# Performance work log

Hardware: AMD Instinct MI355X
Metric: run time of the kernel (lower is better)

## Reference

```python
import jax, jax.numpy as jnp
import numpy as np

N, E, B, IN, H = 20000, 50000, 1024, 32, 64

def setup_inputs() -> dict:
    key = jax.random.key(0)
    ks = jax.random.split(key, 32)
    d = {}
    d["x"] = jax.random.normal(ks[0], (N, IN), jnp.float32)
    d["edge_index"] = jax.random.randint(ks[1], (2, E), 0, N)
    d["edge_attr"] = jax.random.uniform(ks[2], (E, 6), dtype=jnp.float32)
    d["batch"] = jnp.sort(jax.random.randint(ks[3], (N,), 0, B))
    d["t"] = jax.random.uniform(ks[4], (B, 1), dtype=jnp.float32)
    d["p"] = jax.random.uniform(ks[5], (B, 1), dtype=jnp.float32)
    d["num_graphs"] = B
    def lin(k, fan_in, shape):
        return jax.random.normal(k, shape, jnp.float32) * (1.0 / np.sqrt(fan_in))
    # lin0: IN -> H
    d["W0"] = lin(ks[6], IN, (IN, H)); d["b0"] = jnp.zeros((H,), jnp.float32)
    # edge MLP: 6 -> 64 -> H*H
    d["We1"] = lin(ks[7], 6, (6, 64)); d["be1"] = jnp.zeros((64,), jnp.float32)
    d["We2"] = lin(ks[8], 64, (64, H * H)); d["be2"] = jnp.zeros((H * H,), jnp.float32)
    # NNConv root weight + bias
    d["Wroot"] = lin(ks[9], H, (H, H)); d["bconv"] = jnp.zeros((H,), jnp.float32)
    # GRU (input H, hidden H), torch layout [3H, *] gate order r,z,n
    d["gru_wih"] = lin(ks[10], H, (3 * H, H)); d["gru_whh"] = lin(ks[11], H, (3 * H, H))
    d["gru_bih"] = jnp.zeros((3 * H,), jnp.float32); d["gru_bhh"] = jnp.zeros((3 * H,), jnp.float32)
    # Set2Set LSTM (input 2H, hidden H), torch layout [4H, *] gate order i,f,g,o
    d["l_wih"] = lin(ks[12], 2 * H, (4 * H, 2 * H)); d["l_whh"] = lin(ks[13], H, (4 * H, H))
    d["l_bih"] = jnp.zeros((4 * H,), jnp.float32); d["l_bhh"] = jnp.zeros((4 * H,), jnp.float32)
    # readout MLP
    d["W1"] = lin(ks[14], 2 * H + 2, (2 * H + 2, H)); d["b1"] = jnp.zeros((H,), jnp.float32)
    d["W2"] = lin(ks[15], H, (H, 64)); d["b2"] = jnp.zeros((64,), jnp.float32)
    d["W3"] = lin(ks[16], 64, (64, 1)); d["b3"] = jnp.zeros((1,), jnp.float32)
    return d


def reference(x, edge_attr, t, p, W0, b0, We1, be1, We2, be2, Wroot, bconv,
              gru_wih, gru_whh, gru_bih, gru_bhh, l_wih, l_whh, l_bih, l_bhh,
              W1, b1, W2, b2, W3, b3, edge_index, batch, num_graphs):
    n_nodes = x.shape[0]
    hdim = W0.shape[1]
    src, dst = edge_index[0], edge_index[1]

    out = jax.nn.relu(x @ W0 + b0)            # [N,H]
    h = out

    # edge MLP -> per-edge weight matrices [E,H,H] (edge_attr is loop-invariant)
    ew = (jax.nn.relu(edge_attr @ We1 + be1) @ We2 + be2).reshape(-1, hdim, hdim)

    for _ in range(4):
        # NNConv: gather source features, per-edge matmul, scatter-add to targets
        msg = jnp.einsum('eh,eho->eo', out[src], ew)                 # [E,H]
        agg = jax.ops.segment_sum(msg, dst, num_segments=n_nodes)    # [N,H]
        m = jax.nn.relu(agg + out @ Wroot + bconv)
        # GRU step (single timestep)
        gi = m @ gru_wih.T + gru_bih
        gh = h @ gru_whh.T + gru_bhh
        ir, iz, inn = jnp.split(gi, 3, axis=-1)
        hr, hz, hn = jnp.split(gh, 3, axis=-1)
        r = jax.nn.sigmoid(ir + hr)
        z = jax.nn.sigmoid(iz + hz)
        nn_ = jnp.tanh(inn + r * hn)
        h = (1.0 - z) * nn_ + z * h
        out = h

    # Set2Set pooling, 3 processing steps
    qh = jnp.zeros((num_graphs, hdim), x.dtype)
    qc = jnp.zeros((num_graphs, hdim), x.dtype)
    q_star = jnp.zeros((num_graphs, 2 * hdim), x.dtype)
    for _ in range(3):
        g = q_star @ l_wih.T + l_bih + qh @ l_whh.T + l_bhh
        gi_, gf_, gg_, go_ = jnp.split(g, 4, axis=-1)
        qc = jax.nn.sigmoid(gf_) * qc + jax.nn.sigmoid(gi_) * jnp.tanh(gg_)
        qh = jax.nn.sigmoid(go_) * jnp.tanh(qc)
        q = qh                                                        # [B,H]
        e = jnp.sum(out * q[batch], axis=-1, keepdims=True)          # [N,1]
        emax = jax.ops.segment_max(e, batch, num_segments=num_graphs)
        a = jnp.exp(e - emax[batch])
        asum = jax.ops.segment_sum(a, batch, num_segments=num_graphs)
        a = a / asum[batch]                                           # segment softmax
        r_ = jax.ops.segment_sum(a * out, batch, num_segments=num_graphs)
        q_star = jnp.concatenate([q, r_], axis=-1)

    feat = jnp.concatenate([q_star, t, p], axis=-1)                   # [B,2H+2]
    y = jax.nn.relu(feat @ W1 + b1)
    y = jax.nn.relu(y @ W2 + b2)
    y = y @ W3 + b3
    return y.reshape(-1)
```

## Files before the change

kernel.cpp:

```cpp
#include <hip/hip_runtime.h>
#include <math.h>

#define N_NODES 20000
#define N_EDGES 50000
#define NB      1024
#define IND     32
#define HDIM    64

typedef __attribute__((ext_vector_type(8))) short bf16x8;
typedef __attribute__((ext_vector_type(4))) float f32x4;

static inline size_t align_up(size_t x, size_t a) { return (x + a - 1) & ~(a - 1); }

__device__ __forceinline__ float sigmoidf_(float x) {
    return 1.0f / (1.0f + __expf(-x));
}
__device__ __forceinline__ float tanhf_(float x) {
    float xc = fminf(fmaxf(x, -15.0f), 15.0f);
    float e = __expf(2.0f * xc);
    return (e - 1.0f) / (e + 1.0f);
}
__device__ __forceinline__ unsigned pk2(float p0, float p1) {
    unsigned u0 = __float_as_uint(p0) + 0x8000u;
    unsigned u1 = __float_as_uint(p1) + 0x8000u;
    return __builtin_amdgcn_perm(u1, u0, 0x07060302u);
}
__device__ __forceinline__ unsigned bf1(float v) {
    return (__float_as_uint(v) + 0x8000u) >> 16;
}

__global__ void k_prep(const float* __restrict__ We2, const float* __restrict__ be2,
                       short* __restrict__ We2b,
                       const float* __restrict__ Wroot, const float* __restrict__ gwhh,
                       const float* __restrict__ gwih,
                       short* __restrict__ WB1h, short* __restrict__ WB1l,
                       short* __restrict__ WB2h, short* __restrict__ WB2l,
                       const float* __restrict__ lwih, const float* __restrict__ lwhh,
                       float* __restrict__ lwihT, float* __restrict__ lwhhT,
                       const int* __restrict__ batch, int* __restrict__ offs,
                       const float* __restrict__ x, const float* __restrict__ W0,
                       const float* __restrict__ b0, float* __restrict__ hbuf,
                       const float* __restrict__ ea, const float* __restrict__ We1,
                       const float* __restrict__ be1, float* __restrict__ re,
                       const int* __restrict__ ei, int* __restrict__ deg) {
    int bid = blockIdx.x, tid = threadIdx.x;
    if (bid < 1040) {
        int idx = bid * 256 + tid;
        int s = idx >> 12;
        int col = idx & 4095;
        int k = col >> 6, o = col & 63;
        float val = (s < 64) ? We2[k * 4096 + s * 64 + o] : be2[k * 64 + o];
        int dst = s * 4096 + (((o >> 4) * 128 + (k >> 5) * 64 + ((k >> 3) & 3) * 16 + (o & 15)) << 3) + (k & 7);
        We2b[dst] = (short)bf1(val);
    } else if (bid < 1152) {
        int idx = (bid - 1040) * 256 + tid;
        if (idx < 28672) {
            bool b1 = idx < 16384;
            int li = b1 ? idx : idx - 16384;
            int j = li & 7, lane = (li >> 3) & 63, c = (li >> 9) & 1, otile = li >> 10;
            int k = c * 32 + (lane >> 4) * 8 + j;
            int o = otile * 16 + (lane & 15);
            float val;
            if (b1) val = (o < 64) ? Wroot[k * 64 + o] : gwhh[(o - 64) * 64 + k];
            else    val = gwih[o * 64 + k];
            unsigned hs = bf1(val);
            float lo = val - __uint_as_float(hs << 16);
            unsigned ls = bf1(lo);
            if (b1) { WB1h[li] = (short)hs; WB1l[li] = (short)ls; }
            else    { WB2h[li] = (short)hs; WB2l[li] = (short)ls; }
        }
    } else if (bid < 1280) {
        int idx = (bid - 1152) * 256 + tid;
        int i = idx >> 8, j = idx & 255;
        lwihT[idx] = lwih[j * 128 + i];
    } else if (bid < 1344) {
        int idx = (bid - 1280) * 256 + tid;
        int i = idx >> 8, j = idx & 255;
        lwhhT[idx] = lwhh[j * 64 + i];
    } else if (bid < 1349) {
        int i = (bid - 1344) * 256 + tid;
        if (i <= NB) {
            int lo = 0, hi = N_NODES;
            while (lo < hi) { int mid = (lo + hi) >> 1; if (batch[mid] < i) lo = mid + 1; else hi = mid; }
            offs[i] = lo;
        }
    } else if (bid < 6349) {
        int w = tid >> 6, j = tid & 63;
        int n = (bid - 1349) * 4 + w;
        float acc = b0[j];
        const float* xr = x + n * IND;
#pragma unroll
        for (int i = 0; i < IND; ++i) acc = fmaf(xr[i], W0[i * 64 + j], acc);
        hbuf[n * 64 + j] = fmaxf(acc, 0.0f);
    } else if (bid < 18849) {
        int w = tid >> 6, j = tid & 63;
        int e = (bid - 6349) * 4 + w;
        if (e < N_EDGES) {
            float acc = be1[j];
            const float* er = ea + e * 6;
#pragma unroll
            for (int i = 0; i < 6; ++i) acc = fmaf(er[i], We1[i * 64 + j], acc);
            re[e * 64 + j] = fmaxf(acc, 0.0f);
        }
    } else {
        int e = (bid - 18849) * 256 + tid;
        if (e < N_EDGES) atomicAdd(&deg[ei[N_EDGES + e]], 1);
    }
}

__global__ void k_scan(const int* __restrict__ deg, int* __restrict__ rowptr, int* __restrict__ cursor) {
    __shared__ int s_w[16];
    int t = threadIdx.x;
    int base = t * 20;
    int v[20]; int s = 0;
#pragma unroll
    for (int i = 0; i < 20; ++i) {
        int idx = base + i;
        v[i] = (idx < N_NODES) ? deg[idx] : 0;
        s += v[i];
    }
    int lane = t & 63, w = t >> 6;
    int inc = s;
#pragma unroll
    for (int off = 1; off < 64; off <<= 1) {
        int o = __shfl_up(inc, off);
        if (lane >= off) inc += o;
    }
    if (lane == 63) s_w[w] = inc;
    __syncthreads();
    if (w == 0 && lane < 16) {
        int x = s_w[lane];
        int xs = x;
#pragma unroll
        for (int off = 1; off < 16; off <<= 1) {
            int o = __shfl_up(xs, off);
            if (lane >= off) xs += o;
        }
        s_w[lane] = xs - x;
    }
    __syncthreads();
    int run = s_w[w] + (inc - s);
#pragma unroll
    for (int i = 0; i < 20; ++i) {
        int idx = base + i;
        if (idx < N_NODES) { rowptr[idx] = run; cursor[idx] = run; }
        else if (idx == N_NODES) rowptr[idx] = run;
        run += v[i];
    }
}

__global__ void k_fill(const int* __restrict__ ei, int* __restrict__ cursor, int* __restrict__ perm) {
    int e = blockIdx.x * 256 + threadIdx.x;
    if (e < N_EDGES) {
        int pos = atomicAdd(&cursor[ei[N_EDGES + e]], 1);
        perm[pos] = e;
    }
}

__launch_bounds__(256, 3)
__global__ void k_msg_mfma(const float* __restrict__ hbuf, const float* __restrict__ reb,
                           const short* __restrict__ We2b, const int* __restrict__ ei,
                           float* __restrict__ msg) {
    __shared__ float s_v[64][64];
    int tid = threadIdx.x;
    int eb = blockIdx.x * 64;
    int lane = tid & 63;
    int w = tid >> 6;
    int l15 = lane & 15, lhi = lane >> 4;

    {
        int se = tid >> 2;
        int sh = tid & 3;
        int ge = eb + se;
        const float* rowp = (ge < N_EDGES) ? (hbuf + (size_t)ei[ge] * 64) : (const float*)0;
#pragma unroll
        for (int rr4 = 0; rr4 < 4; ++rr4) {
            int hb = rr4 * 16 + sh * 4;
            float4 vv = rowp ? *(const float4*)(rowp + hb) : make_float4(0.f, 0.f, 0.f, 0.f);
            s_v[hb + 0][se] = vv.x; s_v[hb + 1][se] = vv.y;
            s_v[hb + 2][se] = vv.z; s_v[hb + 3][se] = vv.w;
        }
    }

    union U { int4 i4; bf16x8 v; };
    U a_re[4][2];
#pragma unroll
    for (int m = 0; m < 4; ++m) {
        int ge = eb + m * 16 + l15;
        if (ge < N_EDGES) {
            const float* rp = reb + (size_t)ge * 64 + lhi * 8;
            float4 x0 = *(const float4*)(rp);
            float4 x1 = *(const float4*)(rp + 4);
            float4 y0 = *(const float4*)(rp + 32);
            float4 y1 = *(const float4*)(rp + 36);
            a_re[m][0].i4 = make_int4(pk2(x0.x, x0.y), pk2(x0.z, x0.w), pk2(x1.x, x1.y), pk2(x1.z, x1.w));
            a_re[m][1].i4 = make_int4(pk2(y0.x, y0.y), pk2(y0.z, y0.w), pk2(y1.x, y1.y), pk2(y1.z, y1.w));
        } else {
            a_re[m][0].i4 = make_int4(0, 0, 0, 0);
            a_re[m][1].i4 = make_int4(0, 0, 0, 0);
        }
    }

    const int4* bp0 = (const int4*)We2b + (w * 128 + lane);
    const int4* bp1 = bp0 + 64;
    int4 Sc0[4], Sc1[4];
#pragma unroll
    for (int j = 0; j < 4; ++j) {
        Sc0[j] = bp0[j * 512];
        Sc1[j] = bp1[j * 512];
    }

    __syncthreads();

    const f32x4 zero4 = {0.f, 0.f, 0.f, 0.f};
    f32x4 macc[4];
#pragma unroll
    for (int m = 0; m < 4; ++m) macc[m] = zero4;

    float4 vv[4], vn[4];
#pragma unroll
    for (int m = 0; m < 4; ++m) vv[m] = *(const float4*)&s_v[0][m * 16 + lhi * 4];

    for (int g = 0; g < 16; ++g) {
#pragma unroll
        for (int j = 0; j < 4; ++j) {
            int s = g * 4 + j;
            int snext = (s < 63) ? (s + 1) : 63;
#pragma unroll
            for (int m = 0; m < 4; ++m)
                vn[m] = *(const float4*)&s_v[snext][m * 16 + lhi * 4];
            U bb0, bb1; bb0.i4 = Sc0[j]; bb1.i4 = Sc1[j];
#pragma unroll
            for (int m = 0; m < 4; ++m) {
                f32x4 t = __builtin_amdgcn_mfma_f32_16x16x32_bf16(a_re[m][0].v, bb0.v, zero4, 0, 0, 0);
                t = __builtin_amdgcn_mfma_f32_16x16x32_bf16(a_re[m][1].v, bb1.v, t, 0, 0, 0);
                macc[m][0] = fmaf(vv[m].x, t[0], macc[m][0]);
                macc[m][1] = fmaf(vv[m].y, t[1], macc[m][1]);
                macc[m][2] = fmaf(vv[m].z, t[2], macc[m][2]);
                macc[m][3] = fmaf(vv[m].w, t[3], macc[m][3]);
            }
            int sload = (s + 4 <= 64) ? (s + 4) : 64;
            Sc0[j] = bp0[sload * 512];
            Sc1[j] = bp1[sload * 512];
#pragma unroll
            for (int m = 0; m < 4; ++m) vv[m] = vn[m];
        }
    }

    {
        U bb0, bb1; bb0.i4 = Sc0[0]; bb1.i4 = Sc1[0];
#pragma unroll
        for (int m = 0; m < 4; ++m) {
            int e = m * 16 + l15;
            U a0, a1;
            a0.i4 = make_int4(
                pk2(s_v[lhi * 8 + 0][e], s_v[lhi * 8 + 1][e]),
                pk2(s_v[lhi * 8 + 2][e], s_v[lhi * 8 + 3][e]),
                pk2(s_v[lhi * 8 + 4][e], s_v[lhi * 8 + 5][e]),
                pk2(s_v[lhi * 8 + 6][e], s_v[lhi * 8 + 7][e]));
            a1.i4 = make_int4(
                pk2(s_v[32 + lhi * 8 + 0][e], s_v[32 + lhi * 8 + 1][e]),
                pk2(s_v[32 + lhi * 8 + 2][e], s_v[32 + lhi * 8 + 3][e]),
                pk2(s_v[32 + lhi * 8 + 4][e], s_v[32 + lhi * 8 + 5][e]),
                pk2(s_v[32 + lhi * 8 + 6][e], s_v[32 + lhi * 8 + 7][e]));
            macc[m] = __builtin_amdgcn_mfma_f32_16x16x32_bf16(a0.v, bb0.v, macc[m], 0, 0, 0);
            macc[m] = __builtin_amdgcn_mfma_f32_16x16x32_bf16(a1.v, bb1.v, macc[m], 0, 0, 0);
        }
    }
    int o = w * 16 + l15;
#pragma unroll
    for (int m = 0; m < 4; ++m) {
#pragma unroll
        for (int r = 0; r < 4; ++r) {
            int el = m * 16 + lhi * 4 + r;
            int ge = eb + el;
            if (ge < N_EDGES) msg[(size_t)ge * 64 + o] = macc[m][r];
        }
    }
}

__launch_bounds__(256, 4)
__global__ void k_node_update(float* __restrict__ hbuf, const float* __restrict__ msg,
                              const int* __restrict__ rowptr, const int* __restrict__ perm,
                              const short* __restrict__ WB1h, const short* __restrict__ WB1l,
                              const short* __restrict__ WB2h, const short* __restrict__ WB2l,
                              const float* __restrict__ bconv, const float* __restrict__ bih,
                              const float* __restrict__ bhh) {
    __shared__ short s_hh[32][72];
    __shared__ short s_hl[32][72];
    __shared__ short s_mh[32][72];
    __shared__ short s_ml[32][72];
    __shared__ float s_agg[32][68];
    int tid = threadIdx.x;
    int nbase = blockIdx.x * 32;
    int lane = tid & 63, w = tid >> 6;
    int l15 = lane & 15, lhi = lane >> 4;

    {
        int nt = tid >> 3, q = tid & 7;
        int n = nbase + nt;
#pragma unroll
        for (int c4 = 0; c4 < 2; ++c4) {
            int col = q * 8 + c4 * 4;
            float4 v = *(const float4*)&hbuf[(size_t)n * 64 + col];
            unsigned h01 = pk2(v.x, v.y), h23 = pk2(v.z, v.w);
            float f0 = __uint_as_float(h01 << 16);
            float f1 = __uint_as_float(h01 & 0xffff0000u);
            float f2 = __uint_as_float(h23 << 16);
            float f3 = __uint_as_float(h23 & 0xffff0000u);
            unsigned l01 = pk2(v.x - f0, v.y - f1), l23 = pk2(v.z - f2, v.w - f3);
            *(unsigned*)&s_hh[nt][col]     = h01;
            *(unsigned*)&s_hh[nt][col + 2] = h23;
            *(unsigned*)&s_hl[nt][col]     = l01;
            *(unsigned*)&s_hl[nt][col + 2] = l23;
        }
        float4 aggv[2];
#pragma unroll
        for (int c4 = 0; c4 < 2; ++c4)
            aggv[c4] = *(const float4*)&bconv[q * 8 + c4 * 4];
        int rs = rowptr[n], rend = rowptr[n + 1];
        for (int qq = rs; qq < rend; ++qq) {
            const float* mrow = msg + (size_t)perm[qq] * 64 + q * 8;
#pragma unroll
            for (int c4 = 0; c4 < 2; ++c4) {
                float4 mv = *(const float4*)&mrow[c4 * 4];
                aggv[c4].x += mv.x; aggv[c4].y += mv.y;
                aggv[c4].z += mv.z; aggv[c4].w += mv.w;
            }
        }
#pragma unroll
        for (int c4 = 0; c4 < 2; ++c4)
            *(float4*)&s_agg[nt][q * 8 + c4 * 4] = aggv[c4];
    }
    __syncthreads();

    union U { int4 i4; bf16x8 v; };
    U ah[2][2], al[2][2];
#pragma unroll
    for (int m = 0; m < 2; ++m)
#pragma unroll
        for (int c = 0; c < 2; ++c) {
            ah[m][c].i4 = *(const int4*)&s_hh[m * 16 + l15][c * 32 + lhi * 8];
            al[m][c].i4 = *(const int4*)&s_hl[m * 16 + l15][c * 32 + lhi * 8];
        }

    const int4* B1h = (const int4*)WB1h;
    const int4* B1l = (const int4*)WB1l;
    const int4* B2h = (const int4*)WB2h;
    const int4* B2l = (const int4*)WB2l;

    f32x4 C0[2], G[3][2], I[3][2];

    {
        int ot = w;
        U bh0, bh1, bl0, bl1;
        bh0.i4 = B1h[(ot * 2 + 0) * 64 + lane];
        bh1.i4 = B1h[(ot * 2 + 1) * 64 + lane];
        bl0.i4 = B1l[(ot * 2 + 0) * 64 + lane];
        bl1.i4 = B1l[(ot * 2 + 1) * 64 + lane];
#pragma unroll
        for (int m = 0; m < 2; ++m) {
            f32x4 c;
#pragma unroll
            for (int r = 0; r < 4; ++r) c[r] = s_agg[m * 16 + lhi * 4 + r][w * 16 + l15];
            c = __builtin_amdgcn_mfma_f32_16x16x32_bf16(ah[m][0].v, bh0.v, c, 0, 0, 0);
            c = __builtin_amdgcn_mfma_f32_16x16x32_bf16(ah[m][1].v, bh1.v, c, 0, 0, 0);
            c = __builtin_amdgcn_mfma_f32_16x16x32_bf16(al[m][0].v, bh0.v, c, 0, 0, 0);
            c = __builtin_amdgcn_mfma_f32_16x16x32_bf16(al[m][1].v, bh1.v, c, 0, 0, 0);
            c = __builtin_amdgcn_mfma_f32_16x16x32_bf16(ah[m][0].v, bl0.v, c, 0, 0, 0);
            c = __builtin_amdgcn_mfma_f32_16x16x32_bf16(ah[m][1].v, bl1.v, c, 0, 0, 0);
            C0[m] = c;
        }
    }
#pragma unroll
    for (int m = 0; m < 2; ++m)
#pragma unroll
        for (int r = 0; r < 4; ++r) {
            float mv = fmaxf(C0[m][r], 0.0f);
            int row = m * 16 + lhi * 4 + r, col = w * 16 + l15;
            unsigned hs = bf1(mv);
            float lof = mv - __uint_as_float(hs << 16);
            s_mh[row][col] = (short)hs;
            s_ml[row][col] = (short)bf1(lof);
        }
#pragma unroll
    for (int p = 1; p < 4; ++p) {
        int ot = p * 4 + w;
        U bh0, bh1, bl0, bl1;
        bh0.i4 = B1h[(ot * 2 + 0) * 64 + lane];
        bh1.i4 = B1h[(ot * 2 + 1) * 64 + lane];
        bl0.i4 = B1l[(ot * 2 + 0) * 64 + lane];
        bl1.i4 = B1l[(ot * 2 + 1) * 64 + lane];
        float bv = bhh[(p - 1) * 64 + w * 16 + l15];
#pragma unroll
        for (int m = 0; m < 2; ++m) {
            f32x4 c = {bv, bv, bv, bv};
            c = __builtin_amdgcn_mfma_f32_16x16x32_bf16(ah[m][0].v, bh0.v, c, 0, 0, 0);
            c = __builtin_amdgcn_mfma_f32_16x16x32_bf16(ah[m][1].v, bh1.v, c, 0, 0, 0);
            c = __builtin_amdgcn_mfma_f32_16x16x32_bf16(al[m][0].v, bh0.v, c, 0, 0, 0);
            c = __builtin_amdgcn_mfma_f32_16x16x32_bf16(al[m][1].v, bh1.v, c, 0, 0, 0);
            c = __builtin_amdgcn_mfma_f32_16x16x32_bf16(ah[m][0].v, bl0.v, c, 0, 0, 0);
            c = __builtin_amdgcn_mfma_f32_16x16x32_bf16(ah[m][1].v, bl1.v, c, 0, 0, 0);
            G[p - 1][m] = c;
        }
    }
    __syncthreads();
    U mh[2][2], ml[2][2];
#pragma unroll
    for (int m = 0; m < 2; ++m)
#pragma unroll
        for (int c = 0; c < 2; ++c) {
            mh[m][c].i4 = *(const int4*)&s_mh[m * 16 + l15][c * 32 + lhi * 8];
            ml[m][c].i4 = *(const int4*)&s_ml[m * 16 + l15][c * 32 + lhi * 8];
        }
#pragma unroll
    for (int p = 0; p < 3; ++p) {
        int ot = p * 4 + w;
        U bh0, bh1, bl0, bl1;
        bh0.i4 = B2h[(ot * 2 + 0) * 64 + lane];
        bh1.i4 = B2h[(ot * 2 + 1) * 64 + lane];
        bl0.i4 = B2l[(ot * 2 + 0) * 64 + lane];
        bl1.i4 = B2l[(ot * 2 + 1) * 64 + lane];
        float bv = bih[p * 64 + w * 16 + l15];
#pragma unroll
        for (int m = 0; m < 2; ++m) {
            f32x4 c = {bv, bv, bv, bv};
            c = __builtin_amdgcn_mfma_f32_16x16x32_bf16(mh[m][0].v, bh0.v, c, 0, 0, 0);
            c = __builtin_amdgcn_mfma_f32_16x16x32_bf16(mh[m][1].v, bh1.v, c, 0, 0, 0);
            c = __builtin_amdgcn_mfma_f32_16x16x32_bf16(ml[m][0].v, bh0.v, c, 0, 0, 0);
            c = __builtin_amdgcn_mfma_f32_16x16x32_bf16(ml[m][1].v, bh1.v, c, 0, 0, 0);
            c = __builtin_amdgcn_mfma_f32_16x16x32_bf16(mh[m][0].v, bl0.v, c, 0, 0, 0);
            c = __builtin_amdgcn_mfma_f32_16x16x32_bf16(mh[m][1].v, bl1.v, c, 0, 0, 0);
            I[p][m] = c;
        }
    }
#pragma unroll
    for (int m = 0; m < 2; ++m)
#pragma unroll
        for (int r = 0; r < 4; ++r) {
            int row = m * 16 + lhi * 4 + r;
            int n = nbase + row;
            int col = w * 16 + l15;
            float hold = __uint_as_float(((unsigned)(unsigned short)s_hh[row][col]) << 16)
                       + __uint_as_float(((unsigned)(unsigned short)s_hl[row][col]) << 16);
            float rg = sigmoidf_(I[0][m][r] + G[0][m][r]);
            float z  = sigmoidf_(I[1][m][r] + G[1][m][r]);
            float nn = tanhf_(I[2][m][r] + rg * G[2][m][r]);
            hbuf[(size_t)n * 64 + col] = (1.0f - z) * nn + z * hold;
        }
}

__launch_bounds__(256)
__global__ void k_set2set(const float* __restrict__ hbuf, const int* __restrict__ offs,
                          const float* __restrict__ t, const float* __restrict__ p,
                          const float* __restrict__ lwihT, const float* __restrict__ lwhhT,
                          const float* __restrict__ l_bih, const float* __restrict__ l_bhh,
                          const float* __restrict__ W1, const float* __restrict__ b1,
                          const float* __restrict__ W2, const float* __restrict__ b2,
                          const float* __restrict__ W3, const float* __restrict__ b3,
                          float* __restrict__ y) {
    __shared__ float s_qs[192];
    __shared__ float s_g[256];
    __shared__ float s_racc[4][64];
    __shared__ float s_m[4], s_l[4];
    __shared__ float s_y[64];
    int b = blockIdx.x;
    int tid = threadIdx.x;
    int w = tid >> 6, lane = tid & 63;
    int s = offs[b], e = offs[b + 1];
    float bi = l_bih[tid] + l_bhh[tid];
    float qc = 0.f;

    if (tid < 192) s_qs[tid] = 0.f;
    __syncthreads();

    for (int iter = 0; iter < 3; ++iter) {
        float g = bi;
#pragma unroll 8
        for (int i = 0; i < 128; ++i) g = fmaf(s_qs[i], lwihT[i * 256 + tid], g);
#pragma unroll 8
        for (int i = 0; i < 64; ++i)  g = fmaf(s_qs[128 + i], lwhhT[i * 256 + tid], g);
        s_g[tid] = g;
        __syncthreads();
        if (w == 0) {
            float ci = sigmoidf_(s_g[lane]);
            float cf = sigmoidf_(s_g[64 + lane]);
            float cg = tanhf_(s_g[128 + lane]);
            float co = sigmoidf_(s_g[192 + lane]);
            qc = cf * qc + ci * cg;
            float qh = co * tanhf_(qc);
            s_qs[lane] = qh;
            s_qs[128 + lane] = qh;
        }
        __syncthreads();
        float qv = s_qs[128 + lane];
        float mx = -1e30f, l = 0.0f, racc = 0.0f;
        for (int n = s + w; n < e; n += 4) {
            float xv = hbuf[(size_t)n * 64 + lane];
            float prod = xv * qv;
#pragma unroll
            for (int off = 32; off > 0; off >>= 1) prod += __shfl_xor(prod, off);
            float mnew = fmaxf(mx, prod);
            float scale = __expf(mx - mnew);
            float wgt = __expf(prod - mnew);
            l = l * scale + wgt;
            racc = racc * scale + wgt * xv;
            mx = mnew;
        }
        s_racc[w][lane] = racc;
        if (lane == 0) { s_m[w] = mx; s_l[w] = l; }
        __syncthreads();
        if (w == 0) {
            float M = fmaxf(fmaxf(s_m[0], s_m[1]), fmaxf(s_m[2], s_m[3]));
            float L = 0.f, R = 0.f;
#pragma unroll
            for (int ww = 0; ww < 4; ++ww) {
                float sc = __expf(s_m[ww] - M);
                L += s_l[ww] * sc;
                R = fmaf(s_racc[ww][lane], sc, R);
            }
            s_qs[64 + lane] = (e > s) ? (R / L) : 0.0f;
        }
        __syncthreads();
    }
    if (w == 0) {
        float acc = b1[lane];
#pragma unroll 8
        for (int i = 0; i < 128; ++i) acc = fmaf(s_qs[i], W1[i * 64 + lane], acc);
        acc = fmaf(t[b], W1[128 * 64 + lane], acc);
        acc = fmaf(p[b], W1[129 * 64 + lane], acc);
        acc = fmaxf(acc, 0.0f);
        s_y[lane] = acc;
        float acc2 = b2[lane];
#pragma unroll 8
        for (int i = 0; i < 64; ++i) acc2 = fmaf(s_y[i], W2[i * 64 + lane], acc2);
        acc2 = fmaxf(acc2, 0.0f);
        float part = acc2 * W3[lane];
#pragma unroll
        for (int off = 32; off > 0; off >>= 1) part += __shfl_xor(part, off);
        if (lane == 0) y[b] = part + b3[0];
    }
}

extern "C" void kernel_launch(void* const* d_in, const int* in_sizes, int n_in,
                              void* d_out, int out_size, void* d_ws, size_t ws_size,
                              hipStream_t stream) {
    const float* x     = (const float*)d_in[0];
    const int*   ei    = (const int*)  d_in[1];
    const float* ea    = (const float*)d_in[2];
    const int*   batch = (const int*)  d_in[3];
    const float* t     = (const float*)d_in[4];
    const float* p     = (const float*)d_in[5];
    const float* W0    = (const float*)d_in[7];
    const float* b0    = (const float*)d_in[8];
    const float* We1   = (const float*)d_in[9];
    const float* be1   = (const float*)d_in[10];
    const float* We2   = (const float*)d_in[11];
    const float* be2   = (const float*)d_in[12];
    const float* Wroot = (const float*)d_in[13];
    const float* bconv = (const float*)d_in[14];
    const float* gwih  = (const float*)d_in[15];
    const float* gwhh  = (const float*)d_in[16];
    const float* gbih  = (const float*)d_in[17];
    const float* gbhh  = (const float*)d_in[18];
    const float* lwih  = (const float*)d_in[19];
    const float* lwhh  = (const float*)d_in[20];
    const float* lbih  = (const float*)d_in[21];
    const float* lbhh  = (const float*)d_in[22];
    const float* W1    = (const float*)d_in[23];
    const float* b1    = (const float*)d_in[24];
    const float* W2    = (const float*)d_in[25];
    const float* b2    = (const float*)d_in[26];
    const float* W3    = (const float*)d_in[27];
    const float* b3    = (const float*)d_in[28];
    float* y = (float*)d_out;

    char* ws = (char*)d_ws;
    size_t off = 0;
    auto alloc = [&](size_t nbytes) {
        void* ptr = (void*)(ws + off);
        off += align_up(nbytes, 256);
        return ptr;
    };
    float* hbuf   = (float*)alloc((size_t)N_NODES * 64 * 4);
    float* reb    = (float*)alloc((size_t)N_EDGES * 64 * 4);
    float* msg    = (float*)alloc((size_t)N_EDGES * 64 * 4);
    short* We2b   = (short*)alloc((size_t)65 * 4096 * 2);
    short* WB1h   = (short*)alloc(16384 * 2);
    short* WB1l   = (short*)alloc(16384 * 2);
    short* WB2h   = (short*)alloc(12288 * 2);
    short* WB2l   = (short*)alloc(12288 * 2);
    float* lwihT  = (float*)alloc(32768 * 4);
    float* lwhhT  = (float*)alloc(16384 * 4);
    int*   offs   = (int*)  alloc((NB + 1) * 4);
    int*   deg    = (int*)  alloc(N_NODES * 4);
    int*   rowptr = (int*)  alloc((N_NODES + 1) * 4);
    int*   cursor = (int*)  alloc(N_NODES * 4);
    int*   perm   = (int*)  alloc(N_EDGES * 4);

    hipMemsetAsync(deg, 0, (size_t)N_NODES * 4, stream);
    k_prep<<<19045, 256, 0, stream>>>(We2, be2, We2b, Wroot, gwhh, gwih,
                                      WB1h, WB1l, WB2h, WB2l,
                                      lwih, lwhh, lwihT, lwhhT, batch, offs,
                                      x, W0, b0, hbuf, ea, We1, be1, reb,
                                      ei, deg);
    k_scan<<<1, 1024, 0, stream>>>(deg, rowptr, cursor);
    k_fill<<<(N_EDGES + 255) / 256, 256, 0, stream>>>(ei, cursor, perm);

    for (int it = 0; it < 4; ++it) {
        k_msg_mfma<<<(N_EDGES + 63) / 64, 256, 0, stream>>>(hbuf, reb, We2b, ei, msg);
        k_node_update<<<N_NODES / 32, 256, 0, stream>>>(hbuf, msg, rowptr, perm,
                                                        WB1h, WB1l, WB2h, WB2l,
                                                        bconv, gbih, gbhh);
    }

    k_set2set<<<NB, 256, 0, stream>>>(hbuf, offs, t, p, lwihT, lwhhT, lbih, lbhh,
                                      W1, b1, W2, b2, W3, b3, y);
}
```

Baseline: 414.6 us.

## Stream We2 weight slabs into LDS via async global_load_lds ring buffer

Replaces the per-wave register prefetch of We2 bf16 B-fragments with asynchronous global-to-LDS DMA into a four-slot per-wave ring, using manual vmcnt/lgkmcnt waits and double-buffered register fragments. It is meant to hide weight-fetch latency and free VGPRs in the message-passing MFMA kernel. In exchange it adds 32KB of LDS per block, which may reduce occupancy, and relies on fragile hand-placed waitcnt sequencing.

New measurement: 415.5 us. Within noise of the previous version (+0.2%).

```diff
diff --git a/kernel.cpp b/kernel.cpp
--- a/kernel.cpp
+++ b/kernel.cpp
@@ -157,16 +157,41 @@
     }
 }
 
+__device__ __forceinline__ void dma_slab_quarter(const int4* gbase, int lane, int4* ldsbase) {
+    __builtin_amdgcn_global_load_lds((const __attribute__((address_space(1))) int4*)(gbase + lane),
+                                     (__attribute__((address_space(3))) int4*)(ldsbase), 16, 0, 0);
+    __builtin_amdgcn_global_load_lds((const __attribute__((address_space(1))) int4*)(gbase + 64 + lane),
+                                     (__attribute__((address_space(3))) int4*)(ldsbase + 64), 16, 0, 0);
+}
+
+#define MSG_STEP_COMPUTE(PP)                                                                        \
+    _Pragma("unroll")                                                                               \
+    for (int m = 0; m < 4; ++m) {                                                                   \
+        f32x4 t = __builtin_amdgcn_mfma_f32_16x16x32_bf16(a_re[m][0].v, B0[PP].v, zero4, 0, 0, 0);  \
+        t = __builtin_amdgcn_mfma_f32_16x16x32_bf16(a_re[m][1].v, B1[PP].v, t, 0, 0, 0);            \
+        macc[m][0] = fmaf(vbuf[PP][m].x, t[0], macc[m][0]);                                         \
+        macc[m][1] = fmaf(vbuf[PP][m].y, t[1], macc[m][1]);                                         \
+        macc[m][2] = fmaf(vbuf[PP][m].z, t[2], macc[m][2]);                                         \
+        macc[m][3] = fmaf(vbuf[PP][m].w, t[3], macc[m][3]);                                         \
+    }
+
 __launch_bounds__(256, 3)
 __global__ void k_msg_mfma(const float* __restrict__ hbuf, const float* __restrict__ reb,
                            const short* __restrict__ We2b, const int* __restrict__ ei,
                            float* __restrict__ msg) {
     __shared__ float s_v[64][64];
+    __shared__ int4 s_bq[4][4][128];
     int tid = threadIdx.x;
     int eb = blockIdx.x * 64;
     int lane = tid & 63;
     int w = tid >> 6;
     int l15 = lane & 15, lhi = lane >> 4;
+
+    const int4* gb = (const int4*)We2b + w * 128;
+
+#pragma unroll
+    for (int r = 0; r < 4; ++r)
+        dma_slab_quarter(gb + r * 512, lane, &s_bq[w][r][0]);
 
     {
         int se = tid >> 2;
@@ -201,15 +226,6 @@
         }
     }
 
-    const int4* bp0 = (const int4*)We2b + (w * 128 + lane);
-    const int4* bp1 = bp0 + 64;
-    int4 Sc0[4], Sc1[4];
-#pragma unroll
-    for (int j = 0; j < 4; ++j) {
-        Sc0[j] = bp0[j * 512];
-        Sc1[j] = bp1[j * 512];
-    }
-
     __syncthreads();
 
     const f32x4 zero4 = {0.f, 0.f, 0.f, 0.f};
@@ -217,38 +233,55 @@
 #pragma unroll
     for (int m = 0; m < 4; ++m) macc[m] = zero4;
 
-    float4 vv[4], vn[4];
-#pragma unroll
-    for (int m = 0; m < 4; ++m) vv[m] = *(const float4*)&s_v[0][m * 16 + lhi * 4];
-
-    for (int g = 0; g < 16; ++g) {
+    U B0[2], B1[2];
+    float4 vbuf[2][4];
+    B0[0].i4 = s_bq[w][0][lane];
+    B1[0].i4 = s_bq[w][0][64 + lane];
+#pragma unroll
+    for (int m = 0; m < 4; ++m) vbuf[0][m] = *(const float4*)&s_v[0][m * 16 + lhi * 4];
+
+    const int4* gdma = gb + 4 * 512;
+
+    for (int g = 0; g < 15; ++g) {
 #pragma unroll
         for (int j = 0; j < 4; ++j) {
-            int s = g * 4 + j;
-            int snext = (s < 63) ? (s + 1) : 63;
-#pragma unroll
-            for (int m = 0; m < 4; ++m)
-                vn[m] = *(const float4*)&s_v[snext][m * 16 + lhi * 4];
-            U bb0, bb1; bb0.i4 = Sc0[j]; bb1.i4 = Sc1[j];
-#pragma unroll
-            for (int m = 0; m < 4; ++m) {
-                f32x4 t = __builtin_amdgcn_mfma_f32_16x16x32_bf16(a_re[m][0].v, bb0.v, zero4, 0, 0, 0);
-                t = __builtin_amdgcn_mfma_f32_16x16x32_bf16(a_re[m][1].v, bb1.v, t, 0, 0, 0);
-                macc[m][0] = fmaf(vv[m].x, t[0], macc[m][0]);
-                macc[m][1] = fmaf(vv[m].y, t[1], macc[m][1]);
-                macc[m][2] = fmaf(vv[m].z, t[2], macc[m][2]);
-                macc[m][3] = fmaf(vv[m].w, t[3], macc[m][3]);
-            }
-            int sload = (s + 4 <= 64) ? (s + 4) : 64;
-            Sc0[j] = bp0[sload * 512];
-            Sc1[j] = bp1[sload * 512];
-#pragma unroll
-            for (int m = 0; m < 4; ++m) vv[m] = vn[m];
-        }
-    }
+            const int p = j & 1, q = p ^ 1;
+            asm volatile("s_waitcnt lgkmcnt(0)" ::: "memory");
+            dma_slab_quarter(gdma, lane, &s_bq[w][j][0]);
+            gdma += 512;
+            asm volatile("s_waitcnt vmcnt(6)" ::: "memory");
+            const int sn = g * 4 + j + 1;
+            B0[q].i4 = s_bq[w][(j + 1) & 3][lane];
+            B1[q].i4 = s_bq[w][(j + 1) & 3][64 + lane];
+#pragma unroll
+            for (int m = 0; m < 4; ++m) vbuf[q][m] = *(const float4*)&s_v[sn][m * 16 + lhi * 4];
+            MSG_STEP_COMPUTE(p)
+        }
+    }
+
+    asm volatile("s_waitcnt lgkmcnt(0)" ::: "memory");
+    dma_slab_quarter(gdma, lane, &s_bq[w][0][0]);
+    asm volatile("s_waitcnt vmcnt(6)" ::: "memory");
+    B0[1].i4 = s_bq[w][1][lane]; B1[1].i4 = s_bq[w][1][64 + lane];
+#pragma unroll
+    for (int m = 0; m < 4; ++m) vbuf[1][m] = *(const float4*)&s_v[61][m * 16 + lhi * 4];
+    MSG_STEP_COMPUTE(0)
+    asm volatile("s_waitcnt vmcnt(4)" ::: "memory");
+    B0[0].i4 = s_bq[w][2][lane]; B1[0].i4 = s_bq[w][2][64 + lane];
+#pragma unroll
+    for (int m = 0; m < 4; ++m) vbuf[0][m] = *(const float4*)&s_v[62][m * 16 + lhi * 4];
+    MSG_STEP_COMPUTE(1)
+    asm volatile("s_waitcnt vmcnt(2)" ::: "memory");
+    B0[1].i4 = s_bq[w][3][lane]; B1[1].i4 = s_bq[w][3][64 + lane];
+#pragma unroll
+    for (int m = 0; m < 4; ++m) vbuf[1][m] = *(const float4*)&s_v[63][m * 16 + lhi * 4];
+    MSG_STEP_COMPUTE(0)
+    asm volatile("s_waitcnt vmcnt(0)" ::: "memory");
+    B0[0].i4 = s_bq[w][0][lane]; B1[0].i4 = s_bq[w][0][64 + lane];
+    MSG_STEP_COMPUTE(1)
+    asm volatile("s_waitcnt lgkmcnt(0)" ::: "memory");
 
     {
-        U bb0, bb1; bb0.i4 = Sc0[0]; bb1.i4 = Sc1[0];
 #pragma unroll
         for (int m = 0; m < 4; ++m) {
             int e = m * 16 + l15;
@@ -263,8 +296,8 @@
                 pk2(s_v[32 + lhi * 8 + 2][e], s_v[32 + lhi * 8 + 3][e]),
                 pk2(s_v[32 + lhi * 8 + 4][e], s_v[32 + lhi * 8 + 5][e]),
                 pk2(s_v[32 + lhi * 8 + 6][e], s_v[32 + lhi * 8 + 7][e]));
-            macc[m] = __builtin_amdgcn_mfma_f32_16x16x32_bf16(a0.v, bb0.v, macc[m], 0, 0, 0);
-            macc[m] = __builtin_amdgcn_mfma_f32_16x16x32_bf16(a1.v, bb1.v, macc[m], 0, 0, 0);
+            macc[m] = __builtin_amdgcn_mfma_f32_16x16x32_bf16(a0.v, B0[0].v, macc[m], 0, 0, 0);
+            macc[m] = __builtin_amdgcn_mfma_f32_16x16x32_bf16(a1.v, B1[0].v, macc[m], 0, 0, 0);
         }
     }
     int o = w * 16 + l15;
```

## Transpose MFMA operands in edge message kernel and stage output through LDS

Applied to the files above, without the earlier changes.

Swaps the A/B operands of the MFMA so each lane's accumulator holds four output channels for one edge, which turns the per-step h-value scaling into a single scalar LDS read per edge instead of a float4. The final message tile is staged through a padded shared buffer, unioned with the input tile, so global writes become coalesced float4 row stores instead of scattered scalar stores. Launch bounds are raised to target 4 blocks per SM. The risks are two extra barriers and possible register spills under the tighter occupancy bound.

New measurement: 412.7 us. No clear change (-0.5%).

```diff
diff --git a/kernel.cpp b/kernel.cpp
--- a/kernel.cpp
+++ b/kernel.cpp
@@ -157,11 +157,25 @@
     }
 }
 
-__launch_bounds__(256, 3)
+#define MSG_STEP_COMPUTE(BB0, BB1, PP)                                                              \
+    _Pragma("unroll")                                                                               \
+    for (int m = 0; m < 4; ++m) {                                                                   \
+        f32x4 tt = __builtin_amdgcn_mfma_f32_16x16x32_bf16(BB0.v, a_re[m][0].v, zero4, 0, 0, 0);    \
+        tt = __builtin_amdgcn_mfma_f32_16x16x32_bf16(BB1.v, a_re[m][1].v, tt, 0, 0, 0);             \
+        macc[m][0] = fmaf(vsc[PP][m], tt[0], macc[m][0]);                                           \
+        macc[m][1] = fmaf(vsc[PP][m], tt[1], macc[m][1]);                                           \
+        macc[m][2] = fmaf(vsc[PP][m], tt[2], macc[m][2]);                                           \
+        macc[m][3] = fmaf(vsc[PP][m], tt[3], macc[m][3]);                                           \
+    }
+
+__launch_bounds__(256, 4)
 __global__ void k_msg_mfma(const float* __restrict__ hbuf, const float* __restrict__ reb,
                            const short* __restrict__ We2b, const int* __restrict__ ei,
                            float* __restrict__ msg) {
-    __shared__ float s_v[64][64];
+    __shared__ union {
+        float v[64][64];
+        float out[64][68];
+    } s_u;
     int tid = threadIdx.x;
     int eb = blockIdx.x * 64;
     int lane = tid & 63;
@@ -177,8 +191,8 @@
         for (int rr4 = 0; rr4 < 4; ++rr4) {
             int hb = rr4 * 16 + sh * 4;
             float4 vv = rowp ? *(const float4*)(rowp + hb) : make_float4(0.f, 0.f, 0.f, 0.f);
-            s_v[hb + 0][se] = vv.x; s_v[hb + 1][se] = vv.y;
-            s_v[hb + 2][se] = vv.z; s_v[hb + 3][se] = vv.w;
+            s_u.v[hb + 0][se] = vv.x; s_u.v[hb + 1][se] = vv.y;
+            s_u.v[hb + 2][se] = vv.z; s_u.v[hb + 3][se] = vv.w;
         }
     }
 
@@ -217,33 +231,23 @@
 #pragma unroll
     for (int m = 0; m < 4; ++m) macc[m] = zero4;
 
-    float4 vv[4], vn[4];
-#pragma unroll
-    for (int m = 0; m < 4; ++m) vv[m] = *(const float4*)&s_v[0][m * 16 + lhi * 4];
+    float vsc[2][4];
+#pragma unroll
+    for (int m = 0; m < 4; ++m) vsc[0][m] = s_u.v[0][m * 16 + l15];
 
     for (int g = 0; g < 16; ++g) {
 #pragma unroll
         for (int j = 0; j < 4; ++j) {
+            const int p = j & 1, q = p ^ 1;
             int s = g * 4 + j;
             int snext = (s < 63) ? (s + 1) : 63;
 #pragma unroll
-            for (int m = 0; m < 4; ++m)
-                vn[m] = *(const float4*)&s_v[snext][m * 16 + lhi * 4];
+            for (int m = 0; m < 4; ++m) vsc[q][m] = s_u.v[snext][m * 16 + l15];
             U bb0, bb1; bb0.i4 = Sc0[j]; bb1.i4 = Sc1[j];
-#pragma unroll
-            for (int m = 0; m < 4; ++m) {
-                f32x4 t = __builtin_amdgcn_mfma_f32_16x16x32_bf16(a_re[m][0].v, bb0.v, zero4, 0, 0, 0);
-                t = __builtin_amdgcn_mfma_f32_16x16x32_bf16(a_re[m][1].v, bb1.v, t, 0, 0, 0);
-                macc[m][0] = fmaf(vv[m].x, t[0], macc[m][0]);
-                macc[m][1] = fmaf(vv[m].y, t[1], macc[m][1]);
-                macc[m][2] = fmaf(vv[m].z, t[2], macc[m][2]);
-                macc[m][3] = fmaf(vv[m].w, t[3], macc[m][3]);
-            }
+            MSG_STEP_COMPUTE(bb0, bb1, p)
             int sload = (s + 4 <= 64) ? (s + 4) : 64;
             Sc0[j] = bp0[sload * 512];
             Sc1[j] = bp1[sload * 512];
-#pragma unroll
-            for (int m = 0; m < 4; ++m) vv[m] = vn[m];
         }
     }
 
@@ -254,27 +258,35 @@
             int e = m * 16 + l15;
             U a0, a1;
             a0.i4 = make_int4(
-                pk2(s_v[lhi * 8 + 0][e], s_v[lhi * 8 + 1][e]),
-                pk2(s_v[lhi * 8 + 2][e], s_v[lhi * 8 + 3][e]),
-                pk2(s_v[lhi * 8 + 4][e], s_v[lhi * 8 + 5][e]),
-                pk2(s_v[lhi * 8 + 6][e], s_v[lhi * 8 + 7][e]));
+                pk2(s_u.v[lhi * 8 + 0][e], s_u.v[lhi * 8 + 1][e]),
+                pk2(s_u.v[lhi * 8 + 2][e], s_u.v[lhi * 8 + 3][e]),
+                pk2(s_u.v[lhi * 8 + 4][e], s_u.v[lhi * 8 + 5][e]),
+                pk2(s_u.v[lhi * 8 + 6][e], s_u.v[lhi * 8 + 7][e]));
             a1.i4 = make_int4(
-                pk2(s_v[32 + lhi * 8 + 0][e], s_v[32 + lhi * 8 + 1][e]),
-                pk2(s_v[32 + lhi * 8 + 2][e], s_v[32 + lhi * 8 + 3][e]),
-                pk2(s_v[32 + lhi * 8 + 4][e], s_v[32 + lhi * 8 + 5][e]),
-                pk2(s_v[32 + lhi * 8 + 6][e], s_v[32 + lhi * 8 + 7][e]));
-            macc[m] = __builtin_amdgcn_mfma_f32_16x16x32_bf16(a0.v, bb0.v, macc[m], 0, 0, 0);
-            macc[m] = __builtin_amdgcn_mfma_f32_16x16x32_bf16(a1.v, bb1.v, macc[m], 0, 0, 0);
-        }
-    }
-    int o = w * 16 + l15;
+                pk2(s_u.v[32 + lhi * 8 + 0][e], s_u.v[32 + lhi * 8 + 1][e]),
+                pk2(s_u.v[32 + lhi * 8 + 2][e], s_u.v[32 + lhi * 8 + 3][e]),
+                pk2(s_u.v[32 + lhi * 8 + 4][e], s_u.v[32 + lhi * 8 + 5][e]),
+                pk2(s_u.v[32 + lhi * 8 + 6][e], s_u.v[32 + lhi * 8 + 7][e]));
+            macc[m] = __builtin_amdgcn_mfma_f32_16x16x32_bf16(bb0.v, a0.v, macc[m], 0, 0, 0);
+            macc[m] = __builtin_amdgcn_mfma_f32_16x16x32_bf16(bb1.v, a1.v, macc[m], 0, 0, 0);
+        }
+    }
+
+    __syncthreads();
 #pragma unroll
     for (int m = 0; m < 4; ++m) {
-#pragma unroll
-        for (int r = 0; r < 4; ++r) {
-            int el = m * 16 + lhi * 4 + r;
-            int ge = eb + el;
-            if (ge < N_EDGES) msg[(size_t)ge * 64 + o] = macc[m][r];
+        *(float4*)&s_u.out[m * 16 + l15][w * 16 + lhi * 4] =
+            make_float4(macc[m][0], macc[m][1], macc[m][2], macc[m][3]);
+    }
+    __syncthreads();
+    {
+        int er = tid >> 2, qc = tid & 3;
+        int ge = eb + er;
+        if (ge < N_EDGES) {
+#pragma unroll
+            for (int i = 0; i < 4; ++i)
+                *(float4*)&msg[(size_t)ge * 64 + qc * 16 + i * 4] =
+                    *(const float4*)&s_u.out[er][qc * 16 + i * 4];
         }
     }
 }
```

## Make edge-message kernel persistent with LDS-resident weight quarter and chunked edges

Applied to the files above, without the earlier changes.

Turns k_msg_mfma into a persistent kernel of 256 blocks. Each block keeps one quarter of the bf16 We2 output columns resident in LDS, loaded asynchronously with global_load_lds, and loops over 192-edge chunks with a stride of 64 chunks. Gathered source-node features are packed to bf16 in LDS, the MFMA operand roles are swapped, and each lane writes float4 messages. The aim is to stop re-streaming the full edge-weight tensor from global memory for every 64-edge block. The cost is occupancy of one block per CU with large LDS use, and the gather is not overlapped with compute.

Result: slower. 550.4 us (+32.8%).

```diff
diff --git a/kernel.cpp b/kernel.cpp
--- a/kernel.cpp
+++ b/kernel.cpp
@@ -6,6 +6,10 @@
 #define NB      1024
 #define IND     32
 #define HDIM    64
+
+#define CHUNK    192
+#define NCHUNK   ((N_EDGES + CHUNK - 1) / CHUNK)
+#define VPSTRIDE 193
 
 typedef __attribute__((ext_vector_type(8))) short bf16x8;
 typedef __attribute__((ext_vector_type(4))) float f32x4;
@@ -157,125 +161,148 @@
     }
 }
 
-__launch_bounds__(256, 3)
+__launch_bounds__(256, 1)
 __global__ void k_msg_mfma(const float* __restrict__ hbuf, const float* __restrict__ reb,
                            const short* __restrict__ We2b, const int* __restrict__ ei,
                            float* __restrict__ msg) {
-    __shared__ float s_v[64][64];
+    __shared__ int4 sW[64 * 128];
+    __shared__ unsigned vpk[32 * VPSTRIDE];
     int tid = threadIdx.x;
-    int eb = blockIdx.x * 64;
-    int lane = tid & 63;
-    int w = tid >> 6;
+    int lane = tid & 63, w = tid >> 6;
     int l15 = lane & 15, lhi = lane >> 4;
-
-    {
-        int se = tid >> 2;
-        int sh = tid & 3;
-        int ge = eb + se;
-        const float* rowp = (ge < N_EDGES) ? (hbuf + (size_t)ei[ge] * 64) : (const float*)0;
-#pragma unroll
-        for (int rr4 = 0; rr4 < 4; ++rr4) {
-            int hb = rr4 * 16 + sh * 4;
-            float4 vv = rowp ? *(const float4*)(rowp + hb) : make_float4(0.f, 0.f, 0.f, 0.f);
-            s_v[hb + 0][se] = vv.x; s_v[hb + 1][se] = vv.y;
-            s_v[hb + 2][se] = vv.z; s_v[hb + 3][se] = vv.w;
-        }
-    }
-
+    int q = blockIdx.x & 3;
+    int jb = blockIdx.x >> 2;
+    int webase = w * 48;
+    int erow = tid >> 4, c4 = tid & 15;
+
+    const int4* gW = (const int4*)We2b;
     union U { int4 i4; bf16x8 v; };
-    U a_re[4][2];
-#pragma unroll
-    for (int m = 0; m < 4; ++m) {
-        int ge = eb + m * 16 + l15;
-        if (ge < N_EDGES) {
-            const float* rp = reb + (size_t)ge * 64 + lhi * 8;
-            float4 x0 = *(const float4*)(rp);
-            float4 x1 = *(const float4*)(rp + 4);
-            float4 y0 = *(const float4*)(rp + 32);
-            float4 y1 = *(const float4*)(rp + 36);
-            a_re[m][0].i4 = make_int4(pk2(x0.x, x0.y), pk2(x0.z, x0.w), pk2(x1.x, x1.y), pk2(x1.z, x1.w));
-            a_re[m][1].i4 = make_int4(pk2(y0.x, y0.y), pk2(y0.z, y0.w), pk2(y1.x, y1.y), pk2(y1.z, y1.w));
-        } else {
-            a_re[m][0].i4 = make_int4(0, 0, 0, 0);
-            a_re[m][1].i4 = make_int4(0, 0, 0, 0);
-        }
-    }
-
-    const int4* bp0 = (const int4*)We2b + (w * 128 + lane);
-    const int4* bp1 = bp0 + 64;
-    int4 Sc0[4], Sc1[4];
-#pragma unroll
-    for (int j = 0; j < 4; ++j) {
-        Sc0[j] = bp0[j * 512];
-        Sc1[j] = bp1[j * 512];
-    }
-
+
+    U bW0, bW1;
+    bW0.i4 = gW[64 * 512 + q * 128 + lane];
+    bW1.i4 = gW[64 * 512 + q * 128 + 64 + lane];
+
+    for (int r = 0; r < 16; ++r) {
+        int s = r * 4 + w;
+        const int4* src = gW + (size_t)s * 512 + q * 128;
+        __builtin_amdgcn_global_load_lds(
+            (const __attribute__((address_space(1))) int4*)(src + lane),
+            (__attribute__((address_space(3))) int4*)&sW[s * 128], 16, 0, 0);
+        __builtin_amdgcn_global_load_lds(
+            (const __attribute__((address_space(1))) int4*)(src + 64 + lane),
+            (__attribute__((address_space(3))) int4*)&sW[s * 128 + 64], 16, 0, 0);
+    }
+
+    float4 vr[12];
+    U a_re[3][2];
+
+    auto stage_load = [&](int cidx) {
+#pragma unroll
+        for (int k = 0; k < 12; ++k) {
+            int ge = cidx * CHUNK + erow + k * 16;
+            if (ge < N_EDGES)
+                vr[k] = *(const float4*)(hbuf + (size_t)ei[ge] * 64 + c4 * 4);
+            else
+                vr[k] = make_float4(0.f, 0.f, 0.f, 0.f);
+        }
+    };
+    auto pack_write = [&]() {
+#pragma unroll
+        for (int k = 0; k < 12; ++k) {
+            int el = erow + k * 16;
+            vpk[(c4 * 2 + 0) * VPSTRIDE + el] = pk2(vr[k].x, vr[k].y);
+            vpk[(c4 * 2 + 1) * VPSTRIDE + el] = pk2(vr[k].z, vr[k].w);
+        }
+    };
+    auto pack_a_re = [&](int cidx) {
+#pragma unroll
+        for (int m = 0; m < 3; ++m) {
+            int ge = cidx * CHUNK + webase + m * 16 + l15;
+            if (ge < N_EDGES) {
+                const float* rp = reb + (size_t)ge * 64 + lhi * 8;
+                float4 x0 = *(const float4*)(rp);
+                float4 x1 = *(const float4*)(rp + 4);
+                float4 y0 = *(const float4*)(rp + 32);
+                float4 y1 = *(const float4*)(rp + 36);
+                a_re[m][0].i4 = make_int4(pk2(x0.x, x0.y), pk2(x0.z, x0.w), pk2(x1.x, x1.y), pk2(x1.z, x1.w));
+                a_re[m][1].i4 = make_int4(pk2(y0.x, y0.y), pk2(y0.z, y0.w), pk2(y1.x, y1.y), pk2(y1.z, y1.w));
+            } else {
+                a_re[m][0].i4 = make_int4(0, 0, 0, 0);
+                a_re[m][1].i4 = make_int4(0, 0, 0, 0);
+            }
+        }
+    };
+
+    stage_load(jb);
+    pack_a_re(jb);
     __syncthreads();
+    pack_write();
+    __syncthreads();
 
     const f32x4 zero4 = {0.f, 0.f, 0.f, 0.f};
-    f32x4 macc[4];
-#pragma unroll
-    for (int m = 0; m < 4; ++m) macc[m] = zero4;
-
-    float4 vv[4], vn[4];
-#pragma unroll
-    for (int m = 0; m < 4; ++m) vv[m] = *(const float4*)&s_v[0][m * 16 + lhi * 4];
-
-    for (int g = 0; g < 16; ++g) {
-#pragma unroll
-        for (int j = 0; j < 4; ++j) {
-            int s = g * 4 + j;
-            int snext = (s < 63) ? (s + 1) : 63;
-#pragma unroll
-            for (int m = 0; m < 4; ++m)
-                vn[m] = *(const float4*)&s_v[snext][m * 16 + lhi * 4];
-            U bb0, bb1; bb0.i4 = Sc0[j]; bb1.i4 = Sc1[j];
-#pragma unroll
-            for (int m = 0; m < 4; ++m) {
-                f32x4 t = __builtin_amdgcn_mfma_f32_16x16x32_bf16(a_re[m][0].v, bb0.v, zero4, 0, 0, 0);
-                t = __builtin_amdgcn_mfma_f32_16x16x32_bf16(a_re[m][1].v, bb1.v, t, 0, 0, 0);
-                macc[m][0] = fmaf(vv[m].x, t[0], macc[m][0]);
-                macc[m][1] = fmaf(vv[m].y, t[1], macc[m][1]);
-                macc[m][2] = fmaf(vv[m].z, t[2], macc[m][2]);
-                macc[m][3] = fmaf(vv[m].w, t[3], macc[m][3]);
+    int c = jb;
+    while (true) {
+        f32x4 macc[3];
+#pragma unroll
+        for (int m = 0; m < 3; ++m) macc[m] = zero4;
+
+#pragma unroll 4
+        for (int sp = 0; sp < 32; ++sp) {
+            U Fa0, Fb0, Fa1, Fb1;
+            Fa0.i4 = sW[(2 * sp) * 128 + lane];
+            Fb0.i4 = sW[(2 * sp) * 128 + 64 + lane];
+            Fa1.i4 = sW[(2 * sp + 1) * 128 + lane];
+            Fb1.i4 = sW[(2 * sp + 1) * 128 + 64 + lane];
+            unsigned uvm[3];
+#pragma unroll
+            for (int m = 0; m < 3; ++m) uvm[m] = vpk[sp * VPSTRIDE + webase + m * 16 + l15];
+#pragma unroll
+            for (int m = 0; m < 3; ++m) {
+                float fe = __uint_as_float(uvm[m] << 16);
+                float fo = __uint_as_float(uvm[m] & 0xffff0000u);
+                f32x4 t0 = __builtin_amdgcn_mfma_f32_16x16x32_bf16(Fa0.v, a_re[m][0].v, zero4, 0, 0, 0);
+                t0 = __builtin_amdgcn_mfma_f32_16x16x32_bf16(Fb0.v, a_re[m][1].v, t0, 0, 0, 0);
+                macc[m][0] = fmaf(fe, t0[0], macc[m][0]);
+                macc[m][1] = fmaf(fe, t0[1], macc[m][1]);
+                macc[m][2] = fmaf(fe, t0[2], macc[m][2]);
+                macc[m][3] = fmaf(fe, t0[3], macc[m][3]);
+                f32x4 t1 = __builtin_amdgcn_mfma_f32_16x16x32_bf16(Fa1.v, a_re[m][0].v, zero4, 0, 0, 0);
+                t1 = __builtin_amdgcn_mfma_f32_16x16x32_bf16(Fb1.v, a_re[m][1].v, t1, 0, 0, 0);
+                macc[m][0] = fmaf(fo, t1[0], macc[m][0]);
+                macc[m][1] = fmaf(fo, t1[1], macc[m][1]);
+                macc[m][2] = fmaf(fo, t1[2], macc[m][2]);
+                macc[m][3] = fmaf(fo, t1[3], macc[m][3]);
             }
-            int sload = (s + 4 <= 64) ? (s + 4) : 64;
-            Sc0[j] = bp0[sload * 512];
-            Sc1[j] = bp1[sload * 512];
-#pragma unroll
-            for (int m = 0; m < 4; ++m) vv[m] = vn[m];
-        }
-    }
-
-    {
-        U bb0, bb1; bb0.i4 = Sc0[0]; bb1.i4 = Sc1[0];
-#pragma unroll
-        for (int m = 0; m < 4; ++m) {
-            int e = m * 16 + l15;
-            U a0, a1;
-            a0.i4 = make_int4(
-                pk2(s_v[lhi * 8 + 0][e], s_v[lhi * 8 + 1][e]),
-                pk2(s_v[lhi * 8 + 2][e], s_v[lhi * 8 + 3][e]),
-                pk2(s_v[lhi * 8 + 4][e], s_v[lhi * 8 + 5][e]),
-                pk2(s_v[lhi * 8 + 6][e], s_v[lhi * 8 + 7][e]));
-            a1.i4 = make_int4(
-                pk2(s_v[32 + lhi * 8 + 0][e], s_v[32 + lhi * 8 + 1][e]),
-                pk2(s_v[32 + lhi * 8 + 2][e], s_v[32 + lhi * 8 + 3][e]),
-                pk2(s_v[32 + lhi * 8 + 4][e], s_v[32 + lhi * 8 + 5][e]),
-                pk2(s_v[32 + lhi * 8 + 6][e], s_v[32 + lhi * 8 + 7][e]));
-            macc[m] = __builtin_amdgcn_mfma_f32_16x16x32_bf16(a0.v, bb0.v, macc[m], 0, 0, 0);
-            macc[m] = __builtin_amdgcn_mfma_f32_16x16x32_bf16(a1.v, bb1.v, macc[m], 0, 0, 0);
-        }
-    }
-    int o = w * 16 + l15;
-#pragma unroll
-    for (int m = 0; m < 4; ++m) {
-#pragma unroll
-        for (int r = 0; r < 4; ++r) {
-            int el = m * 16 + lhi * 4 + r;
-            int ge = eb + el;
-            if (ge < N_EDGES) msg[(size_t)ge * 64 + o] = macc[m][r];
-        }
+        }
+
+#pragma unroll
+        for (int m = 0; m < 3; ++m) {
+            int e = webase + m * 16 + l15;
+            U vb0, vb1;
+            vb0.i4 = make_int4((int)vpk[(lhi * 4 + 0) * VPSTRIDE + e], (int)vpk[(lhi * 4 + 1) * VPSTRIDE + e],
+                               (int)vpk[(lhi * 4 + 2) * VPSTRIDE + e], (int)vpk[(lhi * 4 + 3) * VPSTRIDE + e]);
+            vb1.i4 = make_int4((int)vpk[(16 + lhi * 4 + 0) * VPSTRIDE + e], (int)vpk[(16 + lhi * 4 + 1) * VPSTRIDE + e],
+                               (int)vpk[(16 + lhi * 4 + 2) * VPSTRIDE + e], (int)vpk[(16 + lhi * 4 + 3) * VPSTRIDE + e]);
+            macc[m] = __builtin_amdgcn_mfma_f32_16x16x32_bf16(bW0.v, vb0.v, macc[m], 0, 0, 0);
+            macc[m] = __builtin_amdgcn_mfma_f32_16x16x32_bf16(bW1.v, vb1.v, macc[m], 0, 0, 0);
+        }
+
+#pragma unroll
+        for (int m = 0; m < 3; ++m) {
+            int ge = c * CHUNK + webase + m * 16 + l15;
+            if (ge < N_EDGES)
+                *(float4*)&msg[(size_t)ge * 64 + q * 16 + lhi * 4] =
+                    make_float4(macc[m][0], macc[m][1], macc[m][2], macc[m][3]);
+        }
+
+        int c2 = c + 64;
+        if (c2 >= NCHUNK) break;
+        __syncthreads();
+        stage_load(c2);
+        pack_a_re(c2);
+        pack_write();
+        __syncthreads();
+        c = c2;
     }
 }
 
@@ -608,7 +635,7 @@
     k_fill<<<(N_EDGES + 255) / 256, 256, 0, stream>>>(ei, cursor, perm);
 
     for (int it = 0; it < 4; ++it) {
-        k_msg_mfma<<<(N_EDGES + 63) / 64, 256, 0, stream>>>(hbuf, reb, We2b, ei, msg);
+        k_msg_mfma<<<256, 256, 0, stream>>>(hbuf, reb, We2b, ei, msg);
         k_node_update<<<N_NODES / 32, 256, 0, stream>>>(hbuf, msg, rowptr, perm,
                                                         WB1h, WB1l, WB2h, WB2l,
                                                         bconv, gbih, gbhh);
```
